# Kernel optimization log

Measured on AMD Instinct MI355X. Metric: run time of the kernel, lower is better.

Reference implementation:

```python
import jax, jax.numpy as jnp
import numpy as np

D = 1024

def setup_inputs() -> dict:
    key = jax.random.key(0)
    kx, kw = jax.random.split(key)
    x = jax.random.normal(kx, (4, 2048, D), dtype=jnp.float32)
    # nn.Linear(d, 3d, bias=False): weight [3d, d]; y = x @ W.T
    W = jax.random.normal(kw, (3 * D, D), dtype=jnp.float32) * (1.0 / np.sqrt(D))
    return {"x": x, "W": W}

def reference(x, W):
    d = x.shape[-1]
    qkv = jnp.einsum('bsd,ed->bse', x, W)  # [B,S,3d]
    q, k, v = jnp.split(qkv, 3, axis=2)
    att = jnp.einsum('bqd,bkd->bqk', q, k) * (1.0 / jnp.sqrt(jnp.asarray(d, x.dtype)))
    att = jax.nn.softmax(att, axis=-1)
    y = jnp.einsum('bqk,bkd->bqd', att, v)
    return y
```

## Files before the change

### kernel.cpp

```cpp
#include <hip/hip_runtime.h>
#include <hip/hip_bf16.h>

typedef __attribute__((ext_vector_type(8))) short short8;
typedef __attribute__((ext_vector_type(4))) float f32x4;

typedef unsigned short u16;

__device__ __forceinline__ u16 f32_to_bf16(float f) {
    unsigned int u = __float_as_uint(f);
    u += 0x7fffu + ((u >> 16) & 1u);
    return (u16)(u >> 16);
}

__device__ __forceinline__ void gload16(const u16* g, u16* lds_base) {
    __builtin_amdgcn_global_load_lds(
        (const __attribute__((address_space(1))) void*)g,
        (__attribute__((address_space(3))) void*)lds_base, 16, 0, 0);
}

__device__ __forceinline__ void phase_bar() {
    __builtin_amdgcn_s_barrier();
    __builtin_amdgcn_sched_barrier(0);
}
__device__ __forceinline__ void wait_vm8() {
    asm volatile("s_waitcnt vmcnt(8)" ::: "memory");
    __builtin_amdgcn_sched_barrier(0);
}
__device__ __forceinline__ void wait_vm0() {
    asm volatile("s_waitcnt vmcnt(0)" ::: "memory");
    __builtin_amdgcn_sched_barrier(0);
}

__global__ void cast_inputs(const float* __restrict__ x, u16* __restrict__ Xb,
                            const float* __restrict__ W, u16* __restrict__ Wb,
                            int nx4, int nw4) {
    int i = blockIdx.x * blockDim.x + threadIdx.x;
    const float* in; u16* out; int idx;
    if (i < nx4) { in = x; out = Xb; idx = i; }
    else { idx = i - nx4; if (idx >= nw4) return; in = W; out = Wb; }
    float4 v = ((const float4*)in)[idx];
    ushort4 o;
    o.x = f32_to_bf16(v.x); o.y = f32_to_bf16(v.y);
    o.z = f32_to_bf16(v.z); o.w = f32_to_bf16(v.w);
    ((ushort4*)out)[idx] = o;
}


struct Acc256 { f32x4 acc[8][4]; };

template<int MH>
__device__ __forceinline__ void rd_a(const u16* __restrict__ sA, int wr, int lane,
                                     int lr, short8 (&af)[4][2]) {
#pragma unroll
    for (int a2 = 0; a2 < 4; ++a2) {
        const int row = wr * 128 + MH * 64 + a2 * 16 + lr;
#pragma unroll
        for (int k2 = 0; k2 < 2; ++k2) {
            const int cb = (lane >> 4) + k2 * 4;
            af[a2][k2] = *(const short8*)(sA + row * 64 + ((cb ^ (lr & 7)) * 8));
        }
    }
}

template<int NH>
__device__ __forceinline__ void rd_b(const u16* __restrict__ sB, int wc, int lane,
                                     int lr, short8 (&bf)[2][2]) {
#pragma unroll
    for (int b2 = 0; b2 < 2; ++b2) {
        const int row = wc * 64 + NH * 32 + b2 * 16 + lr;
#pragma unroll
        for (int k2 = 0; k2 < 2; ++k2) {
            const int cb = (lane >> 4) + k2 * 4;
            bf[b2][k2] = *(const short8*)(sB + row * 64 + ((cb ^ (lr & 7)) * 8));
        }
    }
}

template<int MH, int NH>
__device__ __forceinline__ void mm_q(Acc256& fr, const short8 (&af)[4][2],
                                     const short8 (&bf)[2][2]) {
    __builtin_amdgcn_s_setprio(1);
#pragma unroll
    for (int a2 = 0; a2 < 4; ++a2)
#pragma unroll
        for (int b2 = 0; b2 < 2; ++b2)
#pragma unroll
            for (int k2 = 0; k2 < 2; ++k2)
                fr.acc[MH * 4 + a2][NH * 2 + b2] =
                    __builtin_amdgcn_mfma_f32_16x16x32_bf16(
                        af[a2][k2], bf[b2][k2],
                        fr.acc[MH * 4 + a2][NH * 2 + b2], 0, 0, 0);
    __builtin_amdgcn_s_setprio(0);
}

__device__ __forceinline__ void gemm_core_256(
    const u16* __restrict__ A, const u16* __restrict__ Bt,
    int K, int lda, int ldb, int row0, int col0, u16* sm, Acc256& fr)
{
    const int t    = threadIdx.x;
    const int lane = t & 63;
    const int wave = t >> 6;
    const int wr   = wave >> 2;
    const int wc   = wave & 3;
    const int lr   = lane & 15;
    const int srow = lane >> 3;
    const int gc   = (lane & 7) ^ srow;

    const u16* const sA0 = sm;
    const u16* const sA1 = sm + 16384;
    const u16* const sB0 = sm + 32768;
    const u16* const sB1 = sm + 49152;

#pragma unroll
    for (int a = 0; a < 8; ++a)
#pragma unroll
        for (int b = 0; b < 4; ++b)
            fr.acc[a][b] = (f32x4){0.f, 0.f, 0.f, 0.f};

    const u16* aB = A  + (long long)(row0 + wave * 8 + srow) * lda + gc * 8;
    const u16* bB = Bt + (long long)(col0 + wave * 8 + srow) * ldb + gc * 8;
    u16* const sAw = sm + wave * 512;
    u16* const sBw = sm + 32768 + wave * 512;

    auto stageA = [&](int kt) {
        u16* d = sAw + (kt & 1) * 16384;
        const u16* g = aB + kt * 64;
#pragma unroll
        for (int r4 = 0; r4 < 4; ++r4)
            gload16(g + (long long)(r4 * 64) * lda, d + r4 * 4096);
    };
    auto stageB = [&](int kt) {
        u16* d = sBw + (kt & 1) * 16384;
        const u16* g = bB + kt * 64;
#pragma unroll
        for (int r4 = 0; r4 < 4; ++r4)
            gload16(g + (long long)(r4 * 64) * ldb, d + r4 * 4096);
    };

    stageA(0); stageB(0); stageA(1); stageB(1);
    wait_vm8();
    phase_bar();

    const int NI = K >> 7;
    short8 af[4][2], bfa[2][2], bfb[2][2];
#pragma unroll 1
    for (int i = 0; i < NI; ++i) {
        const bool more = (i + 1 < NI);
        const int t2 = 2 * i + 2;

        rd_a<0>(sA0, wr, lane, lr, af);
        rd_b<0>(sB0, wc, lane, lr, bfa);
        phase_bar();
        mm_q<0, 0>(fr, af, bfa);
        phase_bar();

        rd_b<1>(sB0, wc, lane, lr, bfb);
        phase_bar();
        mm_q<0, 1>(fr, af, bfb);
        phase_bar();

        rd_a<1>(sA0, wr, lane, lr, af);
        if (more) stageB(t2);
        phase_bar();
        mm_q<1, 1>(fr, af, bfb);
        phase_bar();

        if (more) stageA(t2);
        phase_bar();
        mm_q<1, 0>(fr, af, bfa);
        if (more) wait_vm8(); else wait_vm0();
        phase_bar();

        rd_a<0>(sA1, wr, lane, lr, af);
        rd_b<0>(sB1, wc, lane, lr, bfa);
        phase_bar();
        mm_q<0, 0>(fr, af, bfa);
        phase_bar();

        rd_b<1>(sB1, wc, lane, lr, bfb);
        phase_bar();
        mm_q<0, 1>(fr, af, bfb);
        phase_bar();

        rd_a<1>(sA1, wr, lane, lr, af);
        if (more) stageB(t2 + 1);
        phase_bar();
        mm_q<1, 1>(fr, af, bfb);
        phase_bar();

        if (more) stageA(t2 + 1);
        phase_bar();
        mm_q<1, 0>(fr, af, bfa);
        if (more) wait_vm8();
        phase_bar();
    }
}


__global__ __launch_bounds__(512, 1) void gemm_qkv(
    const u16* __restrict__ Xb, const u16* __restrict__ Wb,
    u16* __restrict__ QK, u16* __restrict__ VT)
{
    __shared__ u16 sm[65536];
    const int row0 = blockIdx.y * 256;
    const bool isV = blockIdx.x >= 8;
    const int col0 = (isV ? (blockIdx.x - 8) : blockIdx.x) * 256;
    const u16* Bp  = isV ? (Wb + 2048 * 1024) : Wb;

    Acc256 fr;
    gemm_core_256(Xb, Bp, 1024, 1024, 1024, row0, col0, sm, fr);

    const int lane = threadIdx.x & 63;
    const int wave = threadIdx.x >> 6;
    const int wr = wave >> 2, wc = wave & 3;
    const int cr = (lane >> 4) * 4, cc = lane & 15;

    if (!isV) {
#pragma unroll
        for (int a = 0; a < 8; ++a)
#pragma unroll
            for (int b = 0; b < 4; ++b)
#pragma unroll
                for (int r = 0; r < 4; ++r) {
                    int grow = row0 + wr * 128 + a * 16 + cr + r;
                    int gcol = col0 + wc * 64 + b * 16 + cc;
                    QK[(long long)grow * 2048 + gcol] = f32_to_bf16(fr.acc[a][b][r]);
                }
    } else {
#pragma unroll
        for (int a = 0; a < 8; ++a) {
            int grow = row0 + wr * 128 + a * 16 + cr;
            int bz = grow >> 11, s = grow & 2047;
#pragma unroll
            for (int b = 0; b < 4; ++b) {
                int d = col0 + wc * 64 + b * 16 + cc;
                ushort4 o;
                o.x = f32_to_bf16(fr.acc[a][b][0]);
                o.y = f32_to_bf16(fr.acc[a][b][1]);
                o.z = f32_to_bf16(fr.acc[a][b][2]);
                o.w = f32_to_bf16(fr.acc[a][b][3]);
                *(ushort4*)(&VT[((long long)(bz * 1024 + d)) * 2048 + s]) = o;
            }
        }
    }
}

__global__ __launch_bounds__(512, 1) void gemm_s_exp(
    const u16* __restrict__ QK, u16* __restrict__ E, float* __restrict__ l)
{
    __shared__ u16 sm[65536];
    const long long boff = (long long)blockIdx.z * 2048 * 2048;
    const u16* Q  = QK + boff;
    const u16* Kp = QK + boff + 1024;
    u16* Eb = E + boff;
    float* lb = l + (long long)blockIdx.z * 2048;
    const int row0 = blockIdx.y * 256;
    const int col0 = blockIdx.x * 256;

    Acc256 fr;
    gemm_core_256(Q, Kp, 1024, 2048, 2048, row0, col0, sm, fr);

    const int lane = threadIdx.x & 63;
    const int wave = threadIdx.x >> 6;
    const int wr = wave >> 2, wc = wave & 3;
    const int cr = (lane >> 4) * 4, cc = lane & 15;

#pragma unroll
    for (int a = 0; a < 8; ++a) {
        float rs[4] = {0.f, 0.f, 0.f, 0.f};
#pragma unroll
        for (int b = 0; b < 4; ++b)
#pragma unroll
            for (int r = 0; r < 4; ++r) {
                float e = __expf(fr.acc[a][b][r] * 0.03125f);
                rs[r] += e;
                int grow = row0 + wr * 128 + a * 16 + cr + r;
                int gcol = col0 + wc * 64 + b * 16 + cc;
                Eb[(long long)grow * 2048 + gcol] = f32_to_bf16(e);
            }
#pragma unroll
        for (int r = 0; r < 4; ++r) {
#pragma unroll
            for (int m = 1; m < 16; m <<= 1) rs[r] += __shfl_xor(rs[r], m, 64);
            if ((lane & 15) == 0)
                atomicAdd(&lb[row0 + wr * 128 + a * 16 + cr + r], rs[r]);
        }
    }
}


struct Frag128 { f32x4 acc[4][4]; int lane, wm, wn; };

__device__ __forceinline__ void gemm_core_128(
    const u16* __restrict__ A, const u16* __restrict__ Bt, int K, int lda, int ldb,
    int row0, int col0, u16* sA, u16* sB, Frag128& fr)
{
    const int t    = threadIdx.x;
    const int lane = t & 63;
    const int wave = t >> 6;
    fr.lane = lane;
    fr.wm = (wave >> 1) * 64;
    fr.wn = (wave & 1) * 64;
    const int lr = lane & 15;

#pragma unroll
    for (int i = 0; i < 4; ++i)
#pragma unroll
        for (int j = 0; j < 4; ++j)
            fr.acc[i][j] = (f32x4){0.f, 0.f, 0.f, 0.f};

    const int srow = lane >> 3;
    const int gc   = (lane & 7) ^ srow;
    for (int k0 = 0; k0 < K; k0 += 64) {
        __syncthreads();
#pragma unroll
        for (int c = 0; c < 4; ++c) {
            const int rb = c * 32 + wave * 8;
            const int r  = rb + srow;
            gload16(A  + (long long)(row0 + r) * lda + k0 + gc * 8, &sA[rb * 64]);
            gload16(Bt + (long long)(col0 + r) * ldb + k0 + gc * 8, &sB[rb * 64]);
        }
        __syncthreads();

#pragma unroll
        for (int kk = 0; kk < 64; kk += 32) {
            const int cb = (lane >> 4) + (kk >> 3);
            const int sl = (cb ^ (lr & 7)) * 8;
            short8 af[4], bf[4];
#pragma unroll
            for (int i = 0; i < 4; ++i) {
                af[i] = *(const short8*)(&sA[(fr.wm + i * 16 + lr) * 64 + sl]);
                bf[i] = *(const short8*)(&sB[(fr.wn + i * 16 + lr) * 64 + sl]);
            }
#pragma unroll
            for (int i = 0; i < 4; ++i)
#pragma unroll
                for (int j = 0; j < 4; ++j)
                    fr.acc[i][j] = __builtin_amdgcn_mfma_f32_16x16x32_bf16(
                        af[i], bf[j], fr.acc[i][j], 0, 0, 0);
        }
    }
}

__global__ __launch_bounds__(256) void gemm_pv_ts(
    const u16* __restrict__ E, const u16* __restrict__ VT,
    const float* __restrict__ l, float* __restrict__ Y)
{
    __shared__ u16 sA[128 * 64];
    __shared__ u16 sB[128 * 64];
    const u16* VTb = VT + (long long)blockIdx.z * 1024 * 2048;
    const u16* Eb  = E  + (long long)blockIdx.z * 2048 * 2048;
    const float* lb = l + (long long)blockIdx.z * 2048;
    float* Yb = Y + (long long)blockIdx.z * 2048 * 1024;
    const int row0 = blockIdx.y * 128;
    const int col0 = blockIdx.x * 128;
    Frag128 fr;
    gemm_core_128(VTb, Eb, 2048, 2048, 2048, row0, col0, sA, sB, fr);
    const int cr = (fr.lane >> 4) * 4, cc = fr.lane & 15;
#pragma unroll
    for (int j = 0; j < 4; ++j) {
        int q = col0 + fr.wn + j * 16 + cc;
        float inv = 1.0f / lb[q];
#pragma unroll
        for (int i = 0; i < 4; ++i) {
            int d = row0 + fr.wm + i * 16 + cr;
            float4 o = {fr.acc[i][j][0] * inv, fr.acc[i][j][1] * inv,
                        fr.acc[i][j][2] * inv, fr.acc[i][j][3] * inv};
            *(float4*)(&Yb[(long long)q * 1024 + d]) = o;
        }
    }
}

extern "C" void kernel_launch(void* const* d_in, const int* in_sizes, int n_in,
                              void* d_out, int out_size, void* d_ws, size_t ws_size,
                              hipStream_t stream) {
    const float* x = (const float*)d_in[0];
    const float* W = (const float*)d_in[1];
    float* out = (float*)d_out;

    char* ws = (char*)d_ws;
    u16*   Xb = (u16*)(ws);
    u16*   Wb = (u16*)(ws + 16777216LL);
    u16*   QK = (u16*)(ws + 23068672LL);
    u16*   VT = (u16*)(ws + 56623104LL);
    u16*   E  = (u16*)(ws + 73400320LL);
    float* l  = (float*)(ws + 106954752LL);

    hipMemsetAsync(l, 0, 8192 * sizeof(float), stream);

    cast_inputs<<<11264, 256, 0, stream>>>(x, Xb, W, Wb,
                                           8192 * 1024 / 4, 3072 * 1024 / 4);
    gemm_qkv<<<dim3(12, 32, 1), 512, 0, stream>>>(Xb, Wb, QK, VT);
    gemm_s_exp<<<dim3(8, 8, 4), 512, 0, stream>>>(QK, E, l);
    gemm_pv_ts<<<dim3(16, 8, 4), 256, 0, stream>>>(E, VT, l, out);
}
```

Baseline: 243.4 us.

## Use 256x192 tiles in QKV GEMM for better CU fill; fold memset into cast

The QKV projection GEMM moves from 256x256 tiles on a 12x32 grid (384 blocks) to 256x192 tiles on a 16x32 grid (512 blocks). A new 192-column core with its own LDS staging, B-fragment reads and vmcnt waits supports this. The change aims to fill the 256 CUs with whole waves instead of leaving a partial second wave. The separate memset of the softmax row-sum buffer is folded into the cast kernel to remove one launch. In exchange, each tile does less reuse per loaded element, and the epilogue needs a per-column branch to split Q/K stores from transposed V stores.

Result: no change. 240.0 us (-1.4%).

```diff
diff --git a/kernel.cpp b/kernel.cpp
--- a/kernel.cpp
+++ b/kernel.cpp
@@ -26,6 +26,10 @@
     asm volatile("s_waitcnt vmcnt(8)" ::: "memory");
     __builtin_amdgcn_sched_barrier(0);
 }
+__device__ __forceinline__ void wait_vm7() {
+    asm volatile("s_waitcnt vmcnt(7)" ::: "memory");
+    __builtin_amdgcn_sched_barrier(0);
+}
 __device__ __forceinline__ void wait_vm0() {
     asm volatile("s_waitcnt vmcnt(0)" ::: "memory");
     __builtin_amdgcn_sched_barrier(0);
@@ -33,11 +37,17 @@
 
 __global__ void cast_inputs(const float* __restrict__ x, u16* __restrict__ Xb,
                             const float* __restrict__ W, u16* __restrict__ Wb,
-                            int nx4, int nw4) {
+                            float* __restrict__ l,
+                            int nx4, int nw4, int nl) {
     int i = blockIdx.x * blockDim.x + threadIdx.x;
+    if (i >= nx4 + nw4) {
+        int idx = i - (nx4 + nw4);
+        if (idx < nl) l[idx] = 0.f;
+        return;
+    }
     const float* in; u16* out; int idx;
     if (i < nx4) { in = x; out = Xb; idx = i; }
-    else { idx = i - nx4; if (idx >= nw4) return; in = W; out = Wb; }
+    else { idx = i - nx4; in = W; out = Wb; }
     float4 v = ((const float4*)in)[idx];
     ushort4 o;
     o.x = f32_to_bf16(v.x); o.y = f32_to_bf16(v.y);
@@ -47,6 +57,7 @@
 
 
 struct Acc256 { f32x4 acc[8][4]; };
+struct Acc192 { f32x4 acc[8][3]; };
 
 template<int MH>
 __device__ __forceinline__ void rd_a(const u16* __restrict__ sA, int wr, int lane,
@@ -90,6 +101,60 @@
                     __builtin_amdgcn_mfma_f32_16x16x32_bf16(
                         af[a2][k2], bf[b2][k2],
                         fr.acc[MH * 4 + a2][NH * 2 + b2], 0, 0, 0);
+    __builtin_amdgcn_s_setprio(0);
+}
+
+__device__ __forceinline__ void rd_b01(const u16* __restrict__ sB, int wc, int lane,
+                                       int lr, short8 (&bf)[2][2]) {
+#pragma unroll
+    for (int b2 = 0; b2 < 2; ++b2) {
+        const int row = wc * 48 + b2 * 16 + lr;
+#pragma unroll
+        for (int k2 = 0; k2 < 2; ++k2) {
+            const int cb = (lane >> 4) + k2 * 4;
+            bf[b2][k2] = *(const short8*)(sB + row * 64 + ((cb ^ (lr & 7)) * 8));
+        }
+    }
+}
+
+__device__ __forceinline__ void rd_b2(const u16* __restrict__ sB, int wc, int lane,
+                                      int lr, short8 (&bf)[2]) {
+    const int row = wc * 48 + 32 + lr;
+#pragma unroll
+    for (int k2 = 0; k2 < 2; ++k2) {
+        const int cb = (lane >> 4) + k2 * 4;
+        bf[k2] = *(const short8*)(sB + row * 64 + ((cb ^ (lr & 7)) * 8));
+    }
+}
+
+template<int MH>
+__device__ __forceinline__ void mm_b01(Acc192& fr, const short8 (&af)[4][2],
+                                       const short8 (&bf)[2][2]) {
+    __builtin_amdgcn_s_setprio(1);
+#pragma unroll
+    for (int a2 = 0; a2 < 4; ++a2)
+#pragma unroll
+        for (int b2 = 0; b2 < 2; ++b2)
+#pragma unroll
+            for (int k2 = 0; k2 < 2; ++k2)
+                fr.acc[MH * 4 + a2][b2] =
+                    __builtin_amdgcn_mfma_f32_16x16x32_bf16(
+                        af[a2][k2], bf[b2][k2],
+                        fr.acc[MH * 4 + a2][b2], 0, 0, 0);
+    __builtin_amdgcn_s_setprio(0);
+}
+
+template<int MH>
+__device__ __forceinline__ void mm_b2(Acc192& fr, const short8 (&af)[4][2],
+                                      const short8 (&bf)[2]) {
+    __builtin_amdgcn_s_setprio(1);
+#pragma unroll
+    for (int a2 = 0; a2 < 4; ++a2)
+#pragma unroll
+        for (int k2 = 0; k2 < 2; ++k2)
+            fr.acc[MH * 4 + a2][2] =
+                __builtin_amdgcn_mfma_f32_16x16x32_bf16(
+                    af[a2][k2], bf[k2], fr.acc[MH * 4 + a2][2], 0, 0, 0);
     __builtin_amdgcn_s_setprio(0);
 }
 
@@ -196,44 +261,140 @@
     }
 }
 
+__device__ __forceinline__ void gemm_core_192(
+    const u16* __restrict__ A, const u16* __restrict__ Bt,
+    int K, int lda, int ldb, int row0, int col0, u16* sm, Acc192& fr)
+{
+    const int t    = threadIdx.x;
+    const int lane = t & 63;
+    const int wave = t >> 6;
+    const int wr   = wave >> 2;
+    const int wc   = wave & 3;
+    const int lr   = lane & 15;
+    const int srow = lane >> 3;
+    const int gc   = (lane & 7) ^ srow;
+
+    const u16* const sA0 = sm;
+    const u16* const sA1 = sm + 16384;
+    const u16* const sB0 = sm + 32768;
+    const u16* const sB1 = sm + 45056;
+
+#pragma unroll
+    for (int a = 0; a < 8; ++a)
+#pragma unroll
+        for (int b = 0; b < 3; ++b)
+            fr.acc[a][b] = (f32x4){0.f, 0.f, 0.f, 0.f};
+
+    const u16* aB = A  + (long long)(row0 + wave * 8 + srow) * lda + gc * 8;
+    const u16* bB = Bt + (long long)(col0 + wave * 8 + srow) * ldb + gc * 8;
+    u16* const sAw = sm + wave * 512;
+    u16* const sBw = sm + 32768 + wave * 512;
+
+    auto stageA = [&](int kt) {
+        u16* d = sAw + (kt & 1) * 16384;
+        const u16* g = aB + kt * 64;
+#pragma unroll
+        for (int r4 = 0; r4 < 4; ++r4)
+            gload16(g + (long long)(r4 * 64) * lda, d + r4 * 4096);
+    };
+    auto stageB = [&](int kt) {
+        u16* d = sBw + (kt & 1) * 12288;
+        const u16* g = bB + kt * 64;
+#pragma unroll
+        for (int r4 = 0; r4 < 3; ++r4)
+            gload16(g + (long long)(r4 * 64) * ldb, d + r4 * 4096);
+    };
+
+    stageA(0); stageB(0); stageA(1); stageB(1);
+    wait_vm7();
+    phase_bar();
+
+    const int NI = K >> 7;
+    short8 af[4][2], bfa[2][2], bfb[2];
+#pragma unroll 1
+    for (int i = 0; i < NI; ++i) {
+        const bool more = (i + 1 < NI);
+        const int t2 = 2 * i + 2;
+
+        rd_a<0>(sA0, wr, lane, lr, af);
+        rd_b01(sB0, wc, lane, lr, bfa);
+        phase_bar();
+        mm_b01<0>(fr, af, bfa);
+        phase_bar();
+
+        rd_b2(sB0, wc, lane, lr, bfb);
+        phase_bar();
+        mm_b2<0>(fr, af, bfb);
+        phase_bar();
+
+        rd_a<1>(sA0, wr, lane, lr, af);
+        if (more) stageB(t2);
+        phase_bar();
+        mm_b2<1>(fr, af, bfb);
+        phase_bar();
+
+        if (more) stageA(t2);
+        phase_bar();
+        mm_b01<1>(fr, af, bfa);
+        if (more) wait_vm7(); else wait_vm0();
+        phase_bar();
+
+        rd_a<0>(sA1, wr, lane, lr, af);
+        rd_b01(sB1, wc, lane, lr, bfa);
+        phase_bar();
+        mm_b01<0>(fr, af, bfa);
+        phase_bar();
+
+        rd_b2(sB1, wc, lane, lr, bfb);
+        phase_bar();
+        mm_b2<0>(fr, af, bfb);
+        phase_bar();
+
+        rd_a<1>(sA1, wr, lane, lr, af);
+        if (more) stageB(t2 + 1);
+        phase_bar();
+        mm_b2<1>(fr, af, bfb);
+        phase_bar();
+
+        if (more) stageA(t2 + 1);
+        phase_bar();
+        mm_b01<1>(fr, af, bfa);
+        if (more) wait_vm7();
+        phase_bar();
+    }
+}
+
 
 __global__ __launch_bounds__(512, 1) void gemm_qkv(
     const u16* __restrict__ Xb, const u16* __restrict__ Wb,
     u16* __restrict__ QK, u16* __restrict__ VT)
 {
-    __shared__ u16 sm[65536];
+    __shared__ u16 sm[57344];
     const int row0 = blockIdx.y * 256;
-    const bool isV = blockIdx.x >= 8;
-    const int col0 = (isV ? (blockIdx.x - 8) : blockIdx.x) * 256;
-    const u16* Bp  = isV ? (Wb + 2048 * 1024) : Wb;
-
-    Acc256 fr;
-    gemm_core_256(Xb, Bp, 1024, 1024, 1024, row0, col0, sm, fr);
+    const int col0 = blockIdx.x * 192;
+
+    Acc192 fr;
+    gemm_core_192(Xb, Wb, 1024, 1024, 1024, row0, col0, sm, fr);
 
     const int lane = threadIdx.x & 63;
     const int wave = threadIdx.x >> 6;
     const int wr = wave >> 2, wc = wave & 3;
     const int cr = (lane >> 4) * 4, cc = lane & 15;
 
-    if (!isV) {
-#pragma unroll
-        for (int a = 0; a < 8; ++a)
-#pragma unroll
-            for (int b = 0; b < 4; ++b)
-#pragma unroll
-                for (int r = 0; r < 4; ++r) {
-                    int grow = row0 + wr * 128 + a * 16 + cr + r;
-                    int gcol = col0 + wc * 64 + b * 16 + cc;
-                    QK[(long long)grow * 2048 + gcol] = f32_to_bf16(fr.acc[a][b][r]);
-                }
-    } else {
-#pragma unroll
-        for (int a = 0; a < 8; ++a) {
-            int grow = row0 + wr * 128 + a * 16 + cr;
-            int bz = grow >> 11, s = grow & 2047;
-#pragma unroll
-            for (int b = 0; b < 4; ++b) {
-                int d = col0 + wc * 64 + b * 16 + cc;
+#pragma unroll
+    for (int a = 0; a < 8; ++a) {
+        const int grow = row0 + wr * 128 + a * 16 + cr;
+#pragma unroll
+        for (int b = 0; b < 3; ++b) {
+            const int gcol = col0 + wc * 48 + b * 16 + cc;
+            if (gcol < 2048) {
+#pragma unroll
+                for (int r = 0; r < 4; ++r)
+                    QK[(long long)(grow + r) * 2048 + gcol] =
+                        f32_to_bf16(fr.acc[a][b][r]);
+            } else {
+                const int bz = grow >> 11, s = grow & 2047;
+                const int d = gcol - 2048;
                 ushort4 o;
                 o.x = f32_to_bf16(fr.acc[a][b][0]);
                 o.y = f32_to_bf16(fr.acc[a][b][1]);
@@ -386,11 +547,9 @@
     u16*   E  = (u16*)(ws + 73400320LL);
     float* l  = (float*)(ws + 106954752LL);
 
-    hipMemsetAsync(l, 0, 8192 * sizeof(float), stream);
-
-    cast_inputs<<<11264, 256, 0, stream>>>(x, Xb, W, Wb,
-                                           8192 * 1024 / 4, 3072 * 1024 / 4);
-    gemm_qkv<<<dim3(12, 32, 1), 512, 0, stream>>>(Xb, Wb, QK, VT);
+    const int nx4 = 8192 * 1024 / 4, nw4 = 3072 * 1024 / 4;
+    cast_inputs<<<11296, 256, 0, stream>>>(x, Xb, W, Wb, l, nx4, nw4, 8192);
+    gemm_qkv<<<dim3(16, 32, 1), 512, 0, stream>>>(Xb, Wb, QK, VT);
     gemm_s_exp<<<dim3(8, 8, 4), 512, 0, stream>>>(QK, E, l);
     gemm_pv_ts<<<dim3(16, 8, 4), 256, 0, stream>>>(E, VT, l, out);
 }
```
